# Kernel optimization log

Hardware: AMD Instinct MI355X
Metric: run time of the kernel (lower is better)

The kernel has to match this reference:

```python
import jax, jax.numpy as jnp
import numpy as np

N = 100000      # num nodes
E = 1600000     # num edges (avg degree 16)
F_IN = 700      # hardcoded in_feats in build()
H = 128         # args.hidden
EPS = 1e-5      # BatchNorm1d eps


def setup_inputs() -> dict:
    key = jax.random.key(0)
    ks = jax.random.split(key, 12)
    w = lambda k, shape: jax.random.normal(k, shape, dtype=jnp.float32) * 0.05
    return {
        "inputs": jax.random.normal(ks[0], (1, N, F_IN), dtype=jnp.float32),
        "graph": jax.random.randint(ks[1], (1, E, 2), 0, N, dtype=jnp.int32),
        "Wself0": w(ks[2], (F_IN, H)),
        "Wneigh0": w(ks[3], (F_IN, H)),
        "b0": jnp.zeros((H,), jnp.float32),
        "Wself": w(ks[4], (3, H, H)),
        "Wneigh": w(ks[5], (3, H, H)),
        "b": jnp.zeros((3, H), jnp.float32),
        "bn_gamma": jnp.ones((4, H), jnp.float32),
        "bn_beta": jnp.zeros((4, H), jnp.float32),
        "W1": w(ks[6], (H, 64)),
        "b1": jnp.zeros((64,), jnp.float32),
        "bng1": jnp.ones((64,), jnp.float32),
        "bnb1": jnp.zeros((64,), jnp.float32),
        "W2": w(ks[7], (64, 1)),
        "b2": jnp.zeros((1,), jnp.float32),
    }


def _batch_norm(x, g, beta):
    # training-mode BN over node dim (biased variance, as PyTorch normalizes)
    mu = jnp.mean(x, axis=0)
    var = jnp.mean((x - mu) ** 2, axis=0)
    return (x - mu) * jax.lax.rsqrt(var + EPS) * g + beta


def reference(inputs, graph, Wself0, Wneigh0, b0, Wself, Wneigh, b,
              bn_gamma, bn_beta, W1, b1, bng1, bnb1, W2, b2):
    h = inputs[0]                      # [N, F_IN] (squeeze + flatten is a no-op)
    edges = graph[0]                   # [E, 2]
    src, dst = edges[:, 0], edges[:, 1]
    deg = jax.ops.segment_sum(jnp.ones((E,), jnp.float32), dst, num_segments=N)
    denom = jnp.maximum(deg, 1.0)[:, None]   # DGL clamps zero in-degree

    def sage(x, Ws, Wn, bias):
        # SAGEConv(mean): fc before message passing (linearity => equivalent)
        hn = x @ Wn                                                   # [N, H]
        agg = jax.ops.segment_sum(hn[src], dst, num_segments=N) / denom
        return x @ Ws + agg + bias

    # layer 0: no residual
    h = sage(h, Wself0, Wneigh0, b0)
    h = jax.nn.relu(_batch_norm(h, bn_gamma[0], bn_beta[0]))
    # layers 1..3: BN + residual + relu (dropout = identity in eval)
    for l in range(3):
        pre = h
        h = sage(h, Wself[l], Wneigh[l], b[l])
        h = _batch_norm(h, bn_gamma[l + 1], bn_beta[l + 1])
        h = jax.nn.relu(h + pre)

    z = _batch_norm(h @ W1 + b1, bng1, bnb1)
    z = jax.nn.relu(z)
    out = z @ W2 + b2                  # [N, 1]
    return out.T                       # permute(1,0) -> [1, N]
```

## Files before the change

### kernel.cpp

```cpp
#include <hip/hip_runtime.h>
#include <hip/hip_bf16.h>

#define N_NODES 100000
#define N_EDGES 1600000
#define F_IN    700
#define NKB0    22
#define HDIM    128
#define SCAN_B  256
#define NB_SCAN ((N_NODES + SCAN_B - 1) / SCAN_B)
#define NSHARD  64

typedef _Float16 half8 __attribute__((ext_vector_type(8)));
typedef _Float16 half4 __attribute__((ext_vector_type(4)));
typedef float floatx4 __attribute__((ext_vector_type(4)));

__device__ __forceinline__ void cp16(const void* g, void* l) {
    __builtin_amdgcn_global_load_lds(
        (const __attribute__((address_space(1))) void*)g,
        (__attribute__((address_space(3))) void*)l, 16, 0, 0);
}

__global__ void count_edges(const int* __restrict__ graph, int* __restrict__ cnt) {
    int e = blockIdx.x * blockDim.x + threadIdx.x;
    if (e < N_EDGES) atomicAdd(&cnt[graph[2 * e + 1]], 1);
}

__global__ void scan1(const int* __restrict__ cnt, int* __restrict__ incl,
                      int* __restrict__ blk) {
    __shared__ int s[SCAN_B];
    int tid = threadIdx.x;
    int i = blockIdx.x * SCAN_B + tid;
    s[tid] = (i < N_NODES) ? cnt[i] : 0;
    __syncthreads();
    for (int off = 1; off < SCAN_B; off <<= 1) {
        int t = (tid >= off) ? s[tid - off] : 0;
        __syncthreads();
        s[tid] += t;
        __syncthreads();
    }
    if (i < N_NODES) incl[i] = s[tid];
    if (tid == SCAN_B - 1) blk[blockIdx.x] = s[tid];
}

__global__ void scan2(const int* __restrict__ blk, int* __restrict__ blkoff) {
    __shared__ int s[512];
    int tid = threadIdx.x;
    s[tid] = (tid < NB_SCAN) ? blk[tid] : 0;
    __syncthreads();
    for (int off = 1; off < 512; off <<= 1) {
        int t = (tid >= off) ? s[tid - off] : 0;
        __syncthreads();
        s[tid] += t;
        __syncthreads();
    }
    if (tid < NB_SCAN) blkoff[tid] = (tid == 0) ? 0 : s[tid - 1];
}

__global__ void scan3(const int* __restrict__ incl, const int* __restrict__ blkoff,
                      int* __restrict__ row_ptr) {
    int i = blockIdx.x * SCAN_B + threadIdx.x;
    if (i < N_NODES) {
        row_ptr[i + 1] = incl[i] + blkoff[i >> 8];
        if (i == 0) row_ptr[0] = 0;
    }
}

__global__ void fill_edges(const int* __restrict__ graph, const int* __restrict__ row_ptr,
                           int* __restrict__ cursor, int* __restrict__ esrc) {
    int e = blockIdx.x * blockDim.x + threadIdx.x;
    if (e < N_EDGES) {
        int src = graph[2 * e];
        int dst = graph[2 * e + 1];
        esrc[row_ptr[dst] + atomicAdd(&cursor[dst], 1)] = src;
    }
}

__global__ void build_wtp0(const float* __restrict__ Wn, const float* __restrict__ Ws,
                           _Float16* __restrict__ out) {
    int q = blockIdx.x * blockDim.x + threadIdx.x;
    if (q >= NKB0 * 256 * 4) return;
    int kb = q >> 10;
    int r  = (q >> 2) & 255;
    int cc = q & 3;
    int k0 = kb * 32 + (cc ^ ((r >> 1) & 3)) * 8;
    half8 v;
    #pragma unroll
    for (int e = 0; e < 8; e++) {
        int k = k0 + e;
        float f = 0.0f;
        if (k < F_IN) f = (r < 128) ? Wn[k * 128 + r] : Ws[k * 128 + (r - 128)];
        v[e] = (_Float16)f;
    }
    *(half8*)&out[(size_t)q * 8] = v;
}

__global__ void build_wtpl(const float* __restrict__ Wn, const float* __restrict__ Ws,
                           _Float16* __restrict__ out) {
    int q = blockIdx.x * blockDim.x + threadIdx.x;
    if (q >= 3 * 4 * 256 * 4) return;
    int l = q >> 12;
    int rem = q & 4095;
    int kb = rem >> 10;
    int r  = (rem >> 2) & 255;
    int cc = rem & 3;
    int k0 = kb * 32 + (cc ^ ((r >> 1) & 3)) * 8;
    half8 v;
    #pragma unroll
    for (int e = 0; e < 8; e++) {
        int k = k0 + e;
        float f = (r < 128) ? Wn[l * 16384 + k * 128 + r]
                            : Ws[l * 16384 + k * 128 + (r - 128)];
        v[e] = (_Float16)f;
    }
    *(half8*)&out[(size_t)q * 8] = v;
}

__global__ __launch_bounds__(256) void gemm0_ns(
    const float* __restrict__ A, int M, int K,
    const _Float16* __restrict__ Wtp, const float* __restrict__ bias,
    const float* __restrict__ zbuf,
    _Float16* __restrict__ Cn, _Float16* __restrict__ Cs) {
    __shared__ char sbuf[2][24576];

    int tid = threadIdx.x;
    int wave = tid >> 6, lane = tid & 63;
    int lm = lane & 15, quad = lane >> 4;
    int wm = wave >> 1, wn = wave & 1;
    int bx = blockIdx.x;
    long row0 = (long)(bx >> 1) * 128;
    int nh = bx & 1;

    floatx4 acc[4][4] = {};

    auto stage = [&](int kb, char* buf) {
        #pragma unroll
        for (int pass = 0; pass < 4; pass++) {
            int q = pass * 256 + tid;
            int r = q >> 3, cc = q & 7;
            int ccg = cc ^ (r & 7);
            long grow = row0 + r;
            if (grow >= M) grow = 0;
            int gk = kb * 32 + ccg * 4;
            const float* src = (gk + 4 <= K) ? (A + grow * (long)K + gk) : zbuf;
            cp16(src, buf + pass * 4096 + wave * 1024);
        }
        const _Float16* wsrc = Wtp + (size_t)kb * 8192 + nh * 4096;
        #pragma unroll
        for (int pass = 0; pass < 2; pass++) {
            cp16(wsrc + (size_t)(pass * 256 + tid) * 8,
                 buf + 16384 + pass * 4096 + wave * 1024);
        }
    };

    stage(0, sbuf[0]);

    for (int kb = 0; kb < NKB0; kb++) {
        int p = kb & 1;
        if (kb + 1 < NKB0) {
            stage(kb + 1, sbuf[p ^ 1]);
            asm volatile("s_waitcnt vmcnt(6)\n\ts_barrier" ::: "memory");
        } else {
            asm volatile("s_waitcnt vmcnt(0)\n\ts_barrier" ::: "memory");
        }

        const float* Af = (const float*)sbuf[p];
        const _Float16* Bf = (const _Float16*)(sbuf[p] + 16384);
        half8 af[4];
        #pragma unroll
        for (int i = 0; i < 4; i++) {
            int row = wm * 64 + i * 16 + lm;
            int c0 = (quad * 2) ^ (row & 7);
            int c1 = (quad * 2 + 1) ^ (row & 7);
            floatx4 f0 = *(const floatx4*)&Af[row * 32 + c0 * 4];
            floatx4 f1 = *(const floatx4*)&Af[row * 32 + c1 * 4];
            af[i][0] = (_Float16)f0[0]; af[i][1] = (_Float16)f0[1];
            af[i][2] = (_Float16)f0[2]; af[i][3] = (_Float16)f0[3];
            af[i][4] = (_Float16)f1[0]; af[i][5] = (_Float16)f1[1];
            af[i][6] = (_Float16)f1[2]; af[i][7] = (_Float16)f1[3];
        }
        #pragma unroll
        for (int j = 0; j < 4; j++) {
            int brow = wn * 64 + j * 16 + lm;
            int ch = quad ^ ((brow >> 1) & 3);
            half8 bf = *(const half8*)&Bf[brow * 32 + ch * 8];
            #pragma unroll
            for (int i = 0; i < 4; i++)
                acc[i][j] = __builtin_amdgcn_mfma_f32_16x16x32_f16(af[i], bf, acc[i][j], 0, 0, 0);
        }
        asm volatile("s_waitcnt lgkmcnt(0)\n\ts_barrier" ::: "memory");
    }

    #pragma unroll
    for (int i = 0; i < 4; i++) {
        long r0 = row0 + wm * 64 + i * 16 + quad * 4;
        #pragma unroll
        for (int j = 0; j < 4; j++) {
            int c = wn * 64 + j * 16 + lm;
            if (nh) {
                float badd = bias[c];
                #pragma unroll
                for (int rr = 0; rr < 4; rr++) {
                    long r = r0 + rr;
                    if (r < M) Cs[r * HDIM + c] = (_Float16)(acc[i][j][rr] + badd);
                }
            } else {
                #pragma unroll
                for (int rr = 0; rr < 4; rr++) {
                    long r = r0 + rr;
                    if (r < M) Cn[r * HDIM + c] = (_Float16)acc[i][j][rr];
                }
            }
        }
    }
}

__global__ __launch_bounds__(256) void gemm16_ns(
    const _Float16* __restrict__ A, int M,
    const _Float16* __restrict__ Wtp, const float* __restrict__ bias,
    _Float16* __restrict__ Cn, _Float16* __restrict__ Cs) {
    __shared__ _Float16 sbuf[2][8192];

    int tid = threadIdx.x;
    int wave = tid >> 6, lane = tid & 63;
    int lm = lane & 15, quad = lane >> 4;
    int wm = wave >> 1, wn = wave & 1;
    int bx = blockIdx.x;
    long row0 = (long)(bx >> 1) * 128;
    int nh = bx & 1;

    floatx4 acc[4][4] = {};

    auto stage = [&](int kb, _Float16* buf) {
        #pragma unroll
        for (int pass = 0; pass < 2; pass++) {
            int q = pass * 256 + tid;
            int r = q >> 2, cc = q & 3;
            int ccg = cc ^ ((r >> 1) & 3);
            long grow = row0 + r;
            if (grow >= M) grow = 0;
            cp16(A + grow * (long)HDIM + kb * 32 + ccg * 8,
                 buf + pass * 2048 + wave * 512);
        }
        const _Float16* wsrc = Wtp + (size_t)kb * 8192 + nh * 4096;
        #pragma unroll
        for (int pass = 0; pass < 2; pass++) {
            cp16(wsrc + (size_t)(pass * 256 + tid) * 8,
                 buf + 4096 + pass * 2048 + wave * 512);
        }
    };

    stage(0, sbuf[0]);

    for (int kb = 0; kb < 4; kb++) {
        int p = kb & 1;
        if (kb + 1 < 4) {
            stage(kb + 1, sbuf[p ^ 1]);
            asm volatile("s_waitcnt vmcnt(4)\n\ts_barrier" ::: "memory");
        } else {
            asm volatile("s_waitcnt vmcnt(0)\n\ts_barrier" ::: "memory");
        }

        const _Float16* bp = sbuf[p];
        half8 af[4];
        #pragma unroll
        for (int i = 0; i < 4; i++) {
            int row = wm * 64 + i * 16 + lm;
            int ch = quad ^ ((row >> 1) & 3);
            af[i] = *(const half8*)&bp[row * 32 + ch * 8];
        }
        #pragma unroll
        for (int j = 0; j < 4; j++) {
            int brow = wn * 64 + j * 16 + lm;
            int ch = quad ^ ((brow >> 1) & 3);
            half8 bf = *(const half8*)&bp[4096 + brow * 32 + ch * 8];
            #pragma unroll
            for (int i = 0; i < 4; i++)
                acc[i][j] = __builtin_amdgcn_mfma_f32_16x16x32_f16(af[i], bf, acc[i][j], 0, 0, 0);
        }
        asm volatile("s_waitcnt lgkmcnt(0)\n\ts_barrier" ::: "memory");
    }

    #pragma unroll
    for (int i = 0; i < 4; i++) {
        long r0 = row0 + wm * 64 + i * 16 + quad * 4;
        #pragma unroll
        for (int j = 0; j < 4; j++) {
            int c = wn * 64 + j * 16 + lm;
            if (nh) {
                float badd = bias[c];
                #pragma unroll
                for (int rr = 0; rr < 4; rr++) {
                    long r = r0 + rr;
                    if (r < M) Cs[r * HDIM + c] = (_Float16)(acc[i][j][rr] + badd);
                }
            } else {
                #pragma unroll
                for (int rr = 0; rr < 4; rr++) {
                    long r = r0 + rr;
                    if (r < M) Cn[r * HDIM + c] = (_Float16)acc[i][j][rr];
                }
            }
        }
    }
}

__global__ __launch_bounds__(256) void aggregate_w(
    const _Float16* __restrict__ hn, const int* __restrict__ row_ptr,
    const int* __restrict__ esrc, const _Float16* __restrict__ cs16,
    _Float16* __restrict__ pre16, float* __restrict__ stats) {
    __shared__ float s1[4][HDIM], s2[4][HDIM];
    int tid = threadIdx.x;
    int wave = tid >> 6, lane = tid & 63;
    int n = blockIdx.x * 4 + wave;
    bool valid = (n < N_NODES);
    int eg = lane >> 4;
    int c8 = (lane & 15) * 8;

    float pv[8] = {};
    if (valid) {
        int start = row_ptr[n], end = row_ptr[n + 1];
        float acc[8] = {};
        for (int base = start; base < end; base += 16) {
            #pragma unroll
            for (int u = 0; u < 4; u++) {
                int e = base + u * 4 + eg;
                if (e < end) {
                    int s = esrc[e];
                    half8 v = *(const half8*)&hn[(size_t)s * HDIM + c8];
                    #pragma unroll
                    for (int i = 0; i < 8; i++) acc[i] += (float)v[i];
                }
            }
        }
        #pragma unroll
        for (int i = 0; i < 8; i++) {
            acc[i] += __shfl_xor(acc[i], 16, 64);
            acc[i] += __shfl_xor(acc[i], 32, 64);
        }
        if (eg == 0) {
            float rd = 1.0f / (float)max(end - start, 1);
            half8 sv = *(const half8*)&cs16[(size_t)n * HDIM + c8];
            half8 h;
            #pragma unroll
            for (int i = 0; i < 8; i++) {
                pv[i] = acc[i] * rd + (float)sv[i];
                h[i] = (_Float16)pv[i];
            }
            *(half8*)&pre16[(size_t)n * HDIM + c8] = h;
        }
    }
    if (eg == 0) {
        #pragma unroll
        for (int i = 0; i < 8; i++) {
            float v = valid ? pv[i] : 0.0f;
            s1[wave][c8 + i] = v;
            s2[wave][c8 + i] = v * v;
        }
    }
    __syncthreads();
    if (tid < HDIM) {
        float a = s1[0][tid] + s1[1][tid] + s1[2][tid] + s1[3][tid];
        float b = s2[0][tid] + s2[1][tid] + s2[2][tid] + s2[3][tid];
        float* sh = stats + (size_t)(blockIdx.x & (NSHARD - 1)) * 256;
        atomicAdd(&sh[tid], a);
        atomicAdd(&sh[128 + tid], b);
    }
}

__global__ void bn_apply16(const _Float16* __restrict__ P, const _Float16* __restrict__ res16,
                           _Float16* __restrict__ out16,
                           const float* __restrict__ stats,
                           const float* __restrict__ gamma, const float* __restrict__ beta,
                           int M, int total8, int Cdiv8) {
    __shared__ float ssc[HDIM], ssh[HDIM];
    int tid = threadIdx.x;
    int C = Cdiv8 * 8;
    if (tid < C) {
        float s = 0.0f, s2 = 0.0f;
        #pragma unroll 8
        for (int k = 0; k < NSHARD; k++) {
            s  += stats[k * 256 + tid];
            s2 += stats[k * 256 + 128 + tid];
        }
        float mean = s / (float)M;
        float var = s2 / (float)M - mean * mean;
        float sc = rsqrtf(var + 1e-5f) * gamma[tid];
        ssc[tid] = sc;
        ssh[tid] = beta[tid] - mean * sc;
    }
    __syncthreads();
    for (int f = blockIdx.x * blockDim.x + tid; f < total8;
         f += gridDim.x * blockDim.x) {
        int c8 = (f % Cdiv8) * 8;
        half8 v = *(const half8*)&P[(size_t)f * 8];
        half8 h;
        if (res16) {
            half8 rv = *(const half8*)&res16[(size_t)f * 8];
            #pragma unroll
            for (int i = 0; i < 8; i++) {
                float x = (float)v[i] * ssc[c8 + i] + ssh[c8 + i] + (float)rv[i];
                h[i] = (_Float16)fmaxf(x, 0.0f);
            }
        } else {
            #pragma unroll
            for (int i = 0; i < 8; i++) {
                float x = (float)v[i] * ssc[c8 + i] + ssh[c8 + i];
                h[i] = (_Float16)fmaxf(x, 0.0f);
            }
        }
        *(half8*)&out16[(size_t)f * 8] = h;
    }
}

__global__ __launch_bounds__(256) void mlp_gemm(const _Float16* __restrict__ H,
                                                const float* __restrict__ W1,
                                                const float* __restrict__ b1,
                                                float* __restrict__ Z,
                                                float* __restrict__ stats, int M) {
    __shared__ float hs[64 * 132];
    __shared__ float ws[128 * 64];
    __shared__ float zs1[16][64], zs2[16][64];
    int tid = threadIdx.x;
    int tx = tid & 15;
    int ty = tid >> 4;
    int row0 = blockIdx.x * 64;

    #pragma unroll
    for (int t = 0; t < 8; t++) {
        int f = tid + t * 256;
        int r = f >> 4, c4 = (f & 15) * 4;
        *(float4*)&ws[r * 64 + c4] = *(const float4*)&W1[r * 64 + c4];
    }
    #pragma unroll
    for (int t = 0; t < 4; t++) {
        int f = tid + t * 256;
        int r = f >> 4, c8 = (f & 15) * 8;
        int gr = row0 + r;
        if (gr < M) {
            half8 hv = *(const half8*)&H[(size_t)gr * HDIM + c8];
            #pragma unroll
            for (int i = 0; i < 8; i++) hs[r * 132 + c8 + i] = (float)hv[i];
        } else {
            #pragma unroll
            for (int i = 0; i < 8; i++) hs[r * 132 + c8 + i] = 0.0f;
        }
    }
    __syncthreads();

    float acc[4][4] = {};
    for (int k = 0; k < 128; k++) {
        float a[4];
        #pragma unroll
        for (int i = 0; i < 4; i++) a[i] = hs[(ty * 4 + i) * 132 + k];
        float4 b4 = *(const float4*)&ws[k * 64 + tx * 4];
        #pragma unroll
        for (int i = 0; i < 4; i++) {
            acc[i][0] += a[i] * b4.x; acc[i][1] += a[i] * b4.y;
            acc[i][2] += a[i] * b4.z; acc[i][3] += a[i] * b4.w;
        }
    }
    float4 bb = *(const float4*)&b1[tx * 4];
    float cs[4] = {}, cq[4] = {};
    #pragma unroll
    for (int i = 0; i < 4; i++) {
        int r = row0 + ty * 4 + i;
        if (r < M) {
            float v0 = acc[i][0] + bb.x;
            float v1 = acc[i][1] + bb.y;
            float v2 = acc[i][2] + bb.z;
            float v3 = acc[i][3] + bb.w;
            float4 v = {v0, v1, v2, v3};
            *(float4*)&Z[(size_t)r * 64 + tx * 4] = v;
            cs[0] += v0; cq[0] += v0 * v0;
            cs[1] += v1; cq[1] += v1 * v1;
            cs[2] += v2; cq[2] += v2 * v2;
            cs[3] += v3; cq[3] += v3 * v3;
        }
    }
    #pragma unroll
    for (int j = 0; j < 4; j++) {
        zs1[ty][tx * 4 + j] = cs[j];
        zs2[ty][tx * 4 + j] = cq[j];
    }
    __syncthreads();
    if (tid < 64) {
        float a = 0.0f, b = 0.0f;
        #pragma unroll
        for (int k = 0; k < 16; k++) { a += zs1[k][tid]; b += zs2[k][tid]; }
        float* sh = stats + (size_t)(blockIdx.x & (NSHARD - 1)) * 256;
        atomicAdd(&sh[tid], a);
        atomicAdd(&sh[128 + tid], b);
    }
}

__global__ void final_out(const float* __restrict__ Z,
                          const float* __restrict__ stats,
                          const float* __restrict__ gamma, const float* __restrict__ beta,
                          const float* __restrict__ W2, const float* __restrict__ b2,
                          float* __restrict__ out, int M) {
    __shared__ float ssc[64], ssh[64], sw[64];
    int tid = threadIdx.x;
    if (tid < 64) {
        float s = 0.0f, s2 = 0.0f;
        #pragma unroll 8
        for (int k = 0; k < NSHARD; k++) {
            s  += stats[k * 256 + tid];
            s2 += stats[k * 256 + 128 + tid];
        }
        float mean = s / (float)M;
        float var = s2 / (float)M - mean * mean;
        float sc = rsqrtf(var + 1e-5f) * gamma[tid];
        ssc[tid] = sc;
        ssh[tid] = beta[tid] - mean * sc;
        sw[tid] = W2[tid];
    }
    __syncthreads();
    int n = blockIdx.x * 4 + (tid >> 6);
    int lane = tid & 63;
    if (n >= N_NODES) return;
    float z = Z[(size_t)n * 64 + lane] * ssc[lane] + ssh[lane];
    z = fmaxf(z, 0.0f);
    float v = z * sw[lane];
    #pragma unroll
    for (int off = 32; off >= 1; off >>= 1) v += __shfl_down(v, off, 64);
    if (lane == 0) out[n] = v + b2[0];
}

extern "C" void kernel_launch(void* const* d_in, const int* in_sizes, int n_in,
                              void* d_out, int out_size, void* d_ws, size_t ws_size,
                              hipStream_t stream) {
    const float* X       = (const float*)d_in[0];
    const int*   graph   = (const int*)d_in[1];
    const float* Wself0  = (const float*)d_in[2];
    const float* Wneigh0 = (const float*)d_in[3];
    const float* b0      = (const float*)d_in[4];
    const float* Wself   = (const float*)d_in[5];
    const float* Wneigh  = (const float*)d_in[6];
    const float* bvec    = (const float*)d_in[7];
    const float* bn_g    = (const float*)d_in[8];
    const float* bn_b    = (const float*)d_in[9];
    const float* W1      = (const float*)d_in[10];
    const float* b1      = (const float*)d_in[11];
    const float* bng1    = (const float*)d_in[12];
    const float* bnb1    = (const float*)d_in[13];
    const float* W2      = (const float*)d_in[14];
    const float* b2      = (const float*)d_in[15];
    float* out = (float*)d_out;

    size_t off = 0;
    auto alloc = [&](size_t bytes) {
        void* p = (char*)d_ws + off;
        off += (bytes + 255) & ~(size_t)255;
        return p;
    };
    int* cnt     = (int*)alloc(N_NODES * 4);
    int* cursor  = (int*)alloc(N_NODES * 4);
    int* row_ptr = (int*)alloc((N_NODES + 1) * 4);
    int* incl    = (int*)alloc(N_NODES * 4);
    int* blk     = (int*)alloc(NB_SCAN * 4);
    int* blkoff  = (int*)alloc(NB_SCAN * 4);
    int* esrc    = (int*)alloc((size_t)N_EDGES * 4);
    _Float16* pre16 = (_Float16*)alloc((size_t)N_NODES * HDIM * 2);
    _Float16* cs16  = (_Float16*)alloc((size_t)N_NODES * HDIM * 2);
    _Float16* h16A  = (_Float16*)alloc((size_t)N_NODES * HDIM * 2);
    _Float16* h16B  = (_Float16*)alloc((size_t)N_NODES * HDIM * 2);
    _Float16* hn16  = (_Float16*)alloc((size_t)N_NODES * HDIM * 2);
    float*    Z     = (float*)alloc((size_t)N_NODES * 64 * 4);
    _Float16* Wtp0  = (_Float16*)alloc((size_t)NKB0 * 8192 * 2);
    _Float16* Wtpl  = (_Float16*)alloc((size_t)3 * 4 * 8192 * 2);
    float*    zbuf  = (float*)alloc(256);
    float*    stats = (float*)alloc((size_t)NSHARD * 256 * 4);

    const int EB = (N_EDGES + 255) / 256;
    const int GB = ((N_NODES + 127) / 128) * 2;
    const int AGB = (N_NODES + 3) / 4;
    const size_t STB = (size_t)NSHARD * 256 * 4;
    const int TOT8 = N_NODES * HDIM / 8;

    hipMemsetAsync(cnt, 0, N_NODES * 4, stream);
    hipMemsetAsync(cursor, 0, N_NODES * 4, stream);
    hipMemsetAsync(zbuf, 0, 256, stream);
    count_edges<<<EB, 256, 0, stream>>>(graph, cnt);
    scan1<<<NB_SCAN, SCAN_B, 0, stream>>>(cnt, incl, blk);
    scan2<<<1, 512, 0, stream>>>(blk, blkoff);
    scan3<<<NB_SCAN, SCAN_B, 0, stream>>>(incl, blkoff, row_ptr);
    fill_edges<<<EB, 256, 0, stream>>>(graph, row_ptr, cursor, esrc);

    build_wtp0<<<(NKB0 * 1024 + 255) / 256, 256, 0, stream>>>(Wneigh0, Wself0, Wtp0);
    build_wtpl<<<(3 * 4096 + 255) / 256, 256, 0, stream>>>(Wneigh, Wself, Wtpl);

    _Float16* hc = h16A;
    _Float16* hx = h16B;

    gemm0_ns<<<GB, 256, 0, stream>>>(X, N_NODES, F_IN, Wtp0, b0, zbuf, hn16, cs16);
    hipMemsetAsync(stats, 0, STB, stream);
    aggregate_w<<<AGB, 256, 0, stream>>>(hn16, row_ptr, esrc, cs16, pre16, stats);
    bn_apply16<<<1024, 256, 0, stream>>>(pre16, nullptr, hc, stats,
                                         bn_g, bn_b, N_NODES, TOT8, HDIM / 8);

    for (int l = 0; l < 3; l++) {
        gemm16_ns<<<GB, 256, 0, stream>>>(hc, N_NODES, Wtpl + (size_t)l * 32768,
                                          bvec + l * HDIM, hn16, cs16);
        hipMemsetAsync(stats, 0, STB, stream);
        aggregate_w<<<AGB, 256, 0, stream>>>(hn16, row_ptr, esrc, cs16, pre16, stats);
        bn_apply16<<<1024, 256, 0, stream>>>(pre16, hc, hx, stats,
                                             bn_g + (l + 1) * HDIM,
                                             bn_b + (l + 1) * HDIM, N_NODES,
                                             TOT8, HDIM / 8);
        _Float16* t = hc; hc = hx; hx = t;
    }

    hipMemsetAsync(stats, 0, STB, stream);
    mlp_gemm<<<(N_NODES + 63) / 64, 256, 0, stream>>>(hc, W1, b1, Z, stats, N_NODES);
    final_out<<<AGB, 256, 0, stream>>>(Z, stats, bng1, bnb1, W2, b2,
                                       out, N_NODES);
}
```

Measured before the change: 1.199 ms.

## Merge neighbor/self GEMM halves into one 512-thread block covering all 256 output columns

Before, the fused GEMMs ran as two blocks per 128-row tile, one computing the neighbor projection and one the self projection, so each loaded the same A tile. Now a single 512-thread block (8 waves, 2x4 arrangement) computes all 256 output columns, which halves the A-tile loads from global memory. This matters most for layer 0, where A is the large fp32 700-wide input. In exchange the block uses more LDS and threads, which lowers the number of blocks resident per CU and halves the grid size.

```diff
diff --git a/kernel.cpp b/kernel.cpp
--- a/kernel.cpp
+++ b/kernel.cpp
@@ -115,40 +115,38 @@
     *(half8*)&out[(size_t)q * 8] = v;
 }
 
-__global__ __launch_bounds__(256) void gemm0_ns(
+__global__ __launch_bounds__(512) void gemm0_nu(
     const float* __restrict__ A, int M, int K,
     const _Float16* __restrict__ Wtp, const float* __restrict__ bias,
     const float* __restrict__ zbuf,
     _Float16* __restrict__ Cn, _Float16* __restrict__ Cs) {
-    __shared__ char sbuf[2][24576];
+    __shared__ char sbuf[2][32768];
 
     int tid = threadIdx.x;
     int wave = tid >> 6, lane = tid & 63;
     int lm = lane & 15, quad = lane >> 4;
-    int wm = wave >> 1, wn = wave & 1;
-    int bx = blockIdx.x;
-    long row0 = (long)(bx >> 1) * 128;
-    int nh = bx & 1;
+    int wm = wave >> 2, wn = wave & 3;
+    long row0 = (long)blockIdx.x * 128;
 
     floatx4 acc[4][4] = {};
 
     auto stage = [&](int kb, char* buf) {
         #pragma unroll
-        for (int pass = 0; pass < 4; pass++) {
-            int q = pass * 256 + tid;
+        for (int pass = 0; pass < 2; pass++) {
+            int q = pass * 512 + tid;
             int r = q >> 3, cc = q & 7;
             int ccg = cc ^ (r & 7);
             long grow = row0 + r;
             if (grow >= M) grow = 0;
             int gk = kb * 32 + ccg * 4;
             const float* src = (gk + 4 <= K) ? (A + grow * (long)K + gk) : zbuf;
-            cp16(src, buf + pass * 4096 + wave * 1024);
-        }
-        const _Float16* wsrc = Wtp + (size_t)kb * 8192 + nh * 4096;
+            cp16(src, buf + pass * 8192 + wave * 1024);
+        }
+        const _Float16* wsrc = Wtp + (size_t)kb * 8192;
         #pragma unroll
         for (int pass = 0; pass < 2; pass++) {
-            cp16(wsrc + (size_t)(pass * 256 + tid) * 8,
-                 buf + 16384 + pass * 4096 + wave * 1024);
+            cp16(wsrc + (size_t)(pass * 512 + tid) * 8,
+                 buf + 16384 + pass * 8192 + wave * 1024);
         }
     };
 
@@ -158,7 +156,7 @@
         int p = kb & 1;
         if (kb + 1 < NKB0) {
             stage(kb + 1, sbuf[p ^ 1]);
-            asm volatile("s_waitcnt vmcnt(6)\n\ts_barrier" ::: "memory");
+            asm volatile("s_waitcnt vmcnt(4)\n\ts_barrier" ::: "memory");
         } else {
             asm volatile("s_waitcnt vmcnt(0)\n\ts_barrier" ::: "memory");
         }
@@ -196,12 +194,12 @@
         #pragma unroll
         for (int j = 0; j < 4; j++) {
             int c = wn * 64 + j * 16 + lm;
-            if (nh) {
-                float badd = bias[c];
+            if (c >= 128) {
+                float badd = bias[c - 128];
                 #pragma unroll
                 for (int rr = 0; rr < 4; rr++) {
                     long r = r0 + rr;
-                    if (r < M) Cs[r * HDIM + c] = (_Float16)(acc[i][j][rr] + badd);
+                    if (r < M) Cs[r * HDIM + (c - 128)] = (_Float16)(acc[i][j][rr] + badd);
                 }
             } else {
                 #pragma unroll
@@ -214,38 +212,34 @@
     }
 }
 
-__global__ __launch_bounds__(256) void gemm16_ns(
+__global__ __launch_bounds__(512) void gemm16_nu(
     const _Float16* __restrict__ A, int M,
     const _Float16* __restrict__ Wtp, const float* __restrict__ bias,
     _Float16* __restrict__ Cn, _Float16* __restrict__ Cs) {
-    __shared__ _Float16 sbuf[2][8192];
+    __shared__ _Float16 sbuf[2][12288];
 
     int tid = threadIdx.x;
     int wave = tid >> 6, lane = tid & 63;
     int lm = lane & 15, quad = lane >> 4;
-    int wm = wave >> 1, wn = wave & 1;
-    int bx = blockIdx.x;
-    long row0 = (long)(bx >> 1) * 128;
-    int nh = bx & 1;
+    int wm = wave >> 2, wn = wave & 3;
+    long row0 = (long)blockIdx.x * 128;
 
     floatx4 acc[4][4] = {};
 
     auto stage = [&](int kb, _Float16* buf) {
-        #pragma unroll
-        for (int pass = 0; pass < 2; pass++) {
-            int q = pass * 256 + tid;
-            int r = q >> 2, cc = q & 3;
+        {
+            int r = tid >> 2, cc = tid & 3;
             int ccg = cc ^ ((r >> 1) & 3);
             long grow = row0 + r;
             if (grow >= M) grow = 0;
             cp16(A + grow * (long)HDIM + kb * 32 + ccg * 8,
-                 buf + pass * 2048 + wave * 512);
-        }
-        const _Float16* wsrc = Wtp + (size_t)kb * 8192 + nh * 4096;
+                 buf + wave * 512);
+        }
+        const _Float16* wsrc = Wtp + (size_t)kb * 8192;
         #pragma unroll
         for (int pass = 0; pass < 2; pass++) {
-            cp16(wsrc + (size_t)(pass * 256 + tid) * 8,
-                 buf + 4096 + pass * 2048 + wave * 512);
+            cp16(wsrc + (size_t)(pass * 512 + tid) * 8,
+                 buf + 4096 + pass * 4096 + wave * 512);
         }
     };
 
@@ -255,7 +249,7 @@
         int p = kb & 1;
         if (kb + 1 < 4) {
             stage(kb + 1, sbuf[p ^ 1]);
-            asm volatile("s_waitcnt vmcnt(4)\n\ts_barrier" ::: "memory");
+            asm volatile("s_waitcnt vmcnt(3)\n\ts_barrier" ::: "memory");
         } else {
             asm volatile("s_waitcnt vmcnt(0)\n\ts_barrier" ::: "memory");
         }
@@ -286,12 +280,12 @@
         #pragma unroll
         for (int j = 0; j < 4; j++) {
             int c = wn * 64 + j * 16 + lm;
-            if (nh) {
-                float badd = bias[c];
+            if (c >= 128) {
+                float badd = bias[c - 128];
                 #pragma unroll
                 for (int rr = 0; rr < 4; rr++) {
                     long r = r0 + rr;
-                    if (r < M) Cs[r * HDIM + c] = (_Float16)(acc[i][j][rr] + badd);
+                    if (r < M) Cs[r * HDIM + (c - 128)] = (_Float16)(acc[i][j][rr] + badd);
                 }
             } else {
                 #pragma unroll
@@ -572,7 +566,7 @@
     float*    stats = (float*)alloc((size_t)NSHARD * 256 * 4);
 
     const int EB = (N_EDGES + 255) / 256;
-    const int GB = ((N_NODES + 127) / 128) * 2;
+    const int GB2 = (N_NODES + 127) / 128;
     const int AGB = (N_NODES + 3) / 4;
     const size_t STB = (size_t)NSHARD * 256 * 4;
     const int TOT8 = N_NODES * HDIM / 8;
@@ -592,15 +586,15 @@
     _Float16* hc = h16A;
     _Float16* hx = h16B;
 
-    gemm0_ns<<<GB, 256, 0, stream>>>(X, N_NODES, F_IN, Wtp0, b0, zbuf, hn16, cs16);
+    gemm0_nu<<<GB2, 512, 0, stream>>>(X, N_NODES, F_IN, Wtp0, b0, zbuf, hn16, cs16);
     hipMemsetAsync(stats, 0, STB, stream);
     aggregate_w<<<AGB, 256, 0, stream>>>(hn16, row_ptr, esrc, cs16, pre16, stats);
     bn_apply16<<<1024, 256, 0, stream>>>(pre16, nullptr, hc, stats,
                                          bn_g, bn_b, N_NODES, TOT8, HDIM / 8);
 
     for (int l = 0; l < 3; l++) {
-        gemm16_ns<<<GB, 256, 0, stream>>>(hc, N_NODES, Wtpl + (size_t)l * 32768,
-                                          bvec + l * HDIM, hn16, cs16);
+        gemm16_nu<<<GB2, 512, 0, stream>>>(hc, N_NODES, Wtpl + (size_t)l * 32768,
+                                           bvec + l * HDIM, hn16, cs16);
         hipMemsetAsync(stats, 0, STB, stream);
         aggregate_w<<<AGB, 256, 0, stream>>>(hn16, row_ptr, esrc, cs16, pre16, stats);
         bn_apply16<<<1024, 256, 0, stream>>>(pre16, hc, hx, stats,
```

Result: no change. 1.179 ms (-1.6%).
